# Performance work log

Measured on AMD Instinct MI355X. Metric: run time of the kernel, lower is better.

## Reference

```python
import jax, jax.numpy as jnp
import numpy as np

B, G, D, H, KD = 32, 512, 128, 4, 32  # batch, graph, embed_dim, n_heads, key_dim=embed//heads
NORM = 1.0 / np.sqrt(KD).astype(np.float32)  # MultiHeadCompat norm_factor = 1/sqrt(key_dim)


def _uniform(k, shape, fan):
    s = 1.0 / np.sqrt(fan).astype(np.float32)
    return jax.random.uniform(k, shape, jnp.float32, -s, s)


def setup_inputs() -> dict:
    key = jax.random.key(0)
    ks = jax.random.split(key, 16)
    inp = {
        "h": jax.random.normal(ks[0], (B, G, D), jnp.float32),
        "pos_pickup": jax.random.randint(ks[1], (B,), 0, G),
        "pos_delivery": jax.random.randint(ks[2], (B,), 0, G),
        "rec": jax.random.randint(ks[3], (B, G), 0, G),
        # compater_insert1 / compater_insert2 projections: (n_heads, input_dim, key_dim)
        "Wq1": _uniform(ks[4], (H, D, KD), KD),
        "Wk1": _uniform(ks[5], (H, D, KD), KD),
        "Wq2": _uniform(ks[6], (H, D, KD), KD),
        "Wk2": _uniform(ks[7], (H, D, KD), KD),
        # agg MLP(16, 32, 32, 1); stored as (in, out) so y = x @ W + b
        "fc1_w": _uniform(ks[8], (16, 32), 16),
        "fc1_b": _uniform(ks[9], (32,), 32),
        "fc2_w": _uniform(ks[10], (32, 32), 32),
        "fc2_b": _uniform(ks[11], (32,), 32),
        "fc3_w": _uniform(ks[12], (32, 1), 32),
        "fc3_b": _uniform(ks[13], (1,), 1),
    }
    return inp


def _compat(qv, hh, Wq, Wk):
    # qv: (B, D) single query node; hh: (B, G, D)
    Q = jnp.einsum('bd,hdk->bhk', qv, Wq)       # (B, H, K)
    K = jnp.einsum('bgd,hdk->bhgk', hh, Wk)     # (B, H, G, K)
    return NORM * jnp.einsum('bhk,bhgk->bgh', Q, K)  # (B, G, H)


def reference(h, pos_pickup, pos_delivery, rec, Wq1, Wk1, Wq2, Wk2,
              fc1_w, fc1_b, fc2_w, fc2_b, fc3_w, fc3_b):
    b, g, d = h.shape
    ar = jnp.arange(b)
    h_pickup = h[ar, pos_pickup]      # (B, D)
    h_delivery = h[ar, pos_delivery]  # (B, D)
    h_neighbour = jnp.take_along_axis(h, rec[:, :, None], axis=1)  # (B, G, D)

    shp = (b, g, g, 4)
    c_pp = jnp.broadcast_to(_compat(h_pickup, h, Wq1, Wk1)[:, :, None, :], shp)
    c_po = jnp.broadcast_to(_compat(h_pickup, h_neighbour, Wq2, Wk2)[:, :, None, :], shp)
    c_dp = jnp.broadcast_to(_compat(h_delivery, h, Wq1, Wk1)[:, None, :, :], shp)
    c_do = jnp.broadcast_to(_compat(h_delivery, h_neighbour, Wq2, Wk2)[:, None, :, :], shp)
    x = jnp.concatenate([c_pp, c_po, c_dp, c_do], axis=-1)  # (B, G, G, 16)

    # agg MLP (dropout p=0.05 is identity at inference)
    x = jax.nn.relu(x @ fc1_w + fc1_b)
    x = jax.nn.relu(x @ fc2_w + fc2_b)
    return (x @ fc3_w + fc3_b)[..., 0]  # (B, G, G)
```

## Files before the change

kernel.cpp:

```cpp
#include <hip/hip_runtime.h>


#define B 32
#define G 512
#define D 128
#define NH 4
#define KD 32
#define NORMF 0.17677669529663687f

#define WS_BIASF 1024
#define WS_W3F   1056
#define WS_P16H  131072
#define WS_Q16H  655360

typedef float v16f __attribute__((ext_vector_type(16)));
typedef float f2v __attribute__((ext_vector_type(2)));
typedef _Float16 v8h __attribute__((ext_vector_type(8)));
typedef _Float16 h2v __attribute__((ext_vector_type(2)));

struct HQ { h2v h[4]; };
struct F2x8 { f2v v[8]; };

__device__ __forceinline__ v8h relu_add(const HQ& p, const HQ& q) {
  const h2v z = {(_Float16)0.0f, (_Float16)0.0f};
  HQ r;
#pragma unroll
  for (int i = 0; i < 4; ++i)
    r.h[i] = __builtin_elementwise_max(p.h[i] + q.h[i], z);
  return __builtin_bit_cast(v8h, r);
}

__global__ __launch_bounds__(256) void stage01(
    const float* __restrict__ h, const int* __restrict__ pp,
    const int* __restrict__ pd, const int* __restrict__ rec,
    const float* __restrict__ Wq1, const float* __restrict__ Wk1,
    const float* __restrict__ Wq2, const float* __restrict__ Wk2,
    const float* __restrict__ fc1_w, const float* __restrict__ fc1_b,
    const float* __restrict__ fc2_w, const float* __restrict__ fc2_b,
    const float* __restrict__ fc3_w,
    float* __restrict__ ws) {
  const int bx = blockIdx.x;
  const int b = bx >> 3, g0 = (bx & 7) * 64;
  const int t = threadIdx.x;

  if (bx == 0 && t < 32) {
    _Float16* wt = (_Float16*)ws;
#pragma unroll
    for (int k = 0; k < 32; ++k) wt[t * 32 + k] = (_Float16)fc2_w[k * 32 + t];
    const int r = t & 15, hf = t >> 4;
    const int n = (r & 3) + 8 * (r >> 2) + 4 * hf;
    ws[WS_BIASF + t] = fc2_b[n];
    ws[WS_W3F + t]   = fc3_w[n];
  }

  __shared__ float hp[D], hd[D];
  __shared__ float qq[4][NH * KD];
  __shared__ float sA[4][NH][D];
  __shared__ float sc[64][17];
  __shared__ float sout[64][33];
  __shared__ float sout2[64][33];

  if (t < 128) {
    hp[t] = h[((size_t)b * G + pp[b]) * D + t];
  } else {
    const int u = t - 128;
    hd[u] = h[((size_t)b * G + pd[b]) * D + u];
  }
  __syncthreads();

  if (t < 128) {
    const int hh = t >> 5, k = t & 31;
    const float* wq1 = Wq1 + hh * D * KD + k;
    const float* wq2 = Wq2 + hh * D * KD + k;
    float s1p = 0.f, s2p = 0.f, s1d = 0.f, s2d = 0.f;
#pragma unroll 8
    for (int d = 0; d < D; ++d) {
      const float w1 = wq1[d * KD], w2 = wq2[d * KD];
      const float xp = hp[d], xd = hd[d];
      s1p = fmaf(xp, w1, s1p);
      s2p = fmaf(xp, w2, s2p);
      s1d = fmaf(xd, w1, s1d);
      s2d = fmaf(xd, w2, s2d);
    }
    qq[0][t] = s1p; qq[1][t] = s2p; qq[2][t] = s1d; qq[3][t] = s2d;
  }
  __syncthreads();

  {
    const int d = t & 127;
    const int h0 = (t >> 7) * 2;
#pragma unroll
    for (int hh = h0; hh < h0 + 2; ++hh) {
      const float* wk1 = Wk1 + hh * D * KD + d * KD;
      const float* wk2 = Wk2 + hh * D * KD + d * KD;
      float apq = 0.f, apo = 0.f, adp = 0.f, ado = 0.f;
#pragma unroll
      for (int k = 0; k < KD; ++k) {
        const float w1 = wk1[k], w2 = wk2[k];
        apq = fmaf(qq[0][hh * 32 + k], w1, apq);
        adp = fmaf(qq[2][hh * 32 + k], w1, adp);
        apo = fmaf(qq[1][hh * 32 + k], w2, apo);
        ado = fmaf(qq[3][hh * 32 + k], w2, ado);
      }
      sA[0][hh][d] = NORMF * apq;
      sA[1][hh][d] = NORMF * apo;
      sA[2][hh][d] = NORMF * adp;
      sA[3][hh][d] = NORMF * ado;
    }
  }
  __syncthreads();

  const int gl = t & 63;
  const int hh = __builtin_amdgcn_readfirstlane(t >> 6);
  const int g = g0 + gl;
  const float4* hg4 = (const float4*)(h + ((size_t)b * G + g) * D);
  const float4* hn4 = (const float4*)(h + ((size_t)b * G + rec[b * G + g]) * D);

  float cpp = 0.f, cpo = 0.f, cdp = 0.f, cdo = 0.f;
#pragma unroll 4
  for (int d4 = 0; d4 < 32; ++d4) {
    const float4 x = hg4[d4], y = hn4[d4];
    const float4 a1 = *(const float4*)&sA[0][hh][4 * d4];
    const float4 a2 = *(const float4*)&sA[1][hh][4 * d4];
    const float4 a3 = *(const float4*)&sA[2][hh][4 * d4];
    const float4 a4 = *(const float4*)&sA[3][hh][4 * d4];
    cpp = fmaf(x.x, a1.x, fmaf(x.y, a1.y, fmaf(x.z, a1.z, fmaf(x.w, a1.w, cpp))));
    cpo = fmaf(y.x, a2.x, fmaf(y.y, a2.y, fmaf(y.z, a2.z, fmaf(y.w, a2.w, cpo))));
    cdp = fmaf(x.x, a3.x, fmaf(x.y, a3.y, fmaf(x.z, a3.z, fmaf(x.w, a3.w, cdp))));
    cdo = fmaf(y.x, a4.x, fmaf(y.y, a4.y, fmaf(y.z, a4.z, fmaf(y.w, a4.w, cdo))));
  }
  sc[gl][hh] = cpp; sc[gl][4 + hh] = cpo; sc[gl][8 + hh] = cdp; sc[gl][12 + hh] = cdo;
  __syncthreads();

  float u[16];
#pragma unroll
  for (int i = 0; i < 16; ++i) u[i] = sc[gl][i];

  float pv[8], qv[8];
#pragma unroll
  for (int jj = 0; jj < 8; ++jj) {
    const int j = hh * 8 + jj;
    float p = 0.f, q = fc1_b[j];
#pragma unroll
    for (int i = 0; i < 8; ++i) {
      p = fmaf(u[i], fc1_w[i * 32 + j], p);
      q = fmaf(u[8 + i], fc1_w[(8 + i) * 32 + j], q);
    }
    pv[jj] = p; qv[jj] = q;
  }

#pragma unroll
  for (int jj = 0; jj < 8; ++jj) {
    sout[gl][hh * 8 + jj]  = pv[jj];
    sout2[gl][hh * 8 + jj] = qv[jj];
  }
  __syncthreads();
  {
    unsigned* dstP = (unsigned*)((unsigned short*)ws + WS_P16H) +
                     ((size_t)b * G + g0) * 16;
    unsigned* dstQ = (unsigned*)((unsigned short*)ws + WS_Q16H) +
                     ((size_t)b * G + g0) * 16;
#pragma unroll
    for (int i = t; i < 1024; i += 256) {
      const int row = i >> 4, c0 = (2 * i) & 31;
      __fp16 __attribute__((ext_vector_type(2))) pk =
          __builtin_amdgcn_cvt_pkrtz(sout[row][c0], sout[row][c0 + 1]);
      dstP[i] = *(const unsigned*)&pk;
      __fp16 __attribute__((ext_vector_type(2))) qk =
          __builtin_amdgcn_cvt_pkrtz(sout2[row][c0], sout2[row][c0 + 1]);
      dstQ[i] = *(const unsigned*)&qk;
    }
  }
}

__global__ __launch_bounds__(256, 2) void mlp_pairs(
    const float* __restrict__ ws, const float* __restrict__ fc3_b,
    float* __restrict__ out) {
  const int b = blockIdx.z;
  const int g1_0 = blockIdx.y * 16;
  const int g2_0 = blockIdx.x * 256;
  const int t = threadIdx.x;
  const int w = t >> 6, l = t & 63;
  const int col = l & 31;
  const int half = l >> 5;
  const int kb = half * 8;

  __shared__ __align__(16) unsigned short sPh[16 * 32];
  {
    const unsigned* Psrc = (const unsigned*)((const unsigned short*)ws + WS_P16H) +
                           ((size_t)b * G + g1_0) * 16;
    ((unsigned*)sPh)[t] = Psrc[t];
  }

  const unsigned short* wt = (const unsigned short*)ws;
  const v8h A0 = __builtin_bit_cast(v8h, *(const uint4*)(wt + col * 32 + kb));
  const v8h A1 = __builtin_bit_cast(v8h, *(const uint4*)(wt + col * 32 + 16 + kb));
  const v16f biasC = *(const v16f*)(ws + WS_BIASF + half * 16);
  const F2x8 w3p = __builtin_bit_cast(F2x8, *(const v16f*)(ws + WS_W3F + half * 16));
  const float b3h = 0.5f * fc3_b[0];

  HQ qlo[2], qhi[2];
#pragma unroll
  for (int c = 0; c < 2; ++c) {
    const unsigned short* qp = (const unsigned short*)ws + WS_Q16H +
        ((size_t)b * G + g2_0 + (2 * w + c) * 32 + col) * 32;
    qlo[c] = __builtin_bit_cast(HQ, *(const uint4*)(qp + kb));
    qhi[c] = __builtin_bit_cast(HQ, *(const uint4*)(qp + 16 + kb));
  }
  __syncthreads();

  const f2v binit = {b3h, 0.f};
  const f2v z2 = {0.f, 0.f};
  float* op = out + (((size_t)b * G + g1_0) * G) + g2_0 + w * 64 + half * 32 + col;
#pragma unroll 4
  for (int i = 0; i < 8; ++i) {
    const int ra = 2 * i, rb = 2 * i + 1;
    const HQ palo = __builtin_bit_cast(HQ, *(const uint4*)(sPh + ra * 32 + kb));
    const HQ pahi = __builtin_bit_cast(HQ, *(const uint4*)(sPh + ra * 32 + 16 + kb));
    const HQ pblo = __builtin_bit_cast(HQ, *(const uint4*)(sPh + rb * 32 + kb));
    const HQ pbhi = __builtin_bit_cast(HQ, *(const uint4*)(sPh + rb * 32 + 16 + kb));

    const v8h Ba0lo = relu_add(palo, qlo[0]);
    const v8h Ba0hi = relu_add(pahi, qhi[0]);
    const v8h Ba1lo = relu_add(palo, qlo[1]);
    const v8h Ba1hi = relu_add(pahi, qhi[1]);
    const v8h Bb0lo = relu_add(pblo, qlo[0]);
    const v8h Bb0hi = relu_add(pbhi, qhi[0]);
    const v8h Bb1lo = relu_add(pblo, qlo[1]);
    const v8h Bb1hi = relu_add(pbhi, qhi[1]);

    v16f aa0 = __builtin_amdgcn_mfma_f32_32x32x16_f16(A0, Ba0lo, biasC, 0, 0, 0);
    v16f aa1 = __builtin_amdgcn_mfma_f32_32x32x16_f16(A0, Ba1lo, biasC, 0, 0, 0);
    v16f ab0 = __builtin_amdgcn_mfma_f32_32x32x16_f16(A0, Bb0lo, biasC, 0, 0, 0);
    v16f ab1 = __builtin_amdgcn_mfma_f32_32x32x16_f16(A0, Bb1lo, biasC, 0, 0, 0);
    aa0 = __builtin_amdgcn_mfma_f32_32x32x16_f16(A1, Ba0hi, aa0, 0, 0, 0);
    aa1 = __builtin_amdgcn_mfma_f32_32x32x16_f16(A1, Ba1hi, aa1, 0, 0, 0);
    ab0 = __builtin_amdgcn_mfma_f32_32x32x16_f16(A1, Bb0hi, ab0, 0, 0, 0);
    ab1 = __builtin_amdgcn_mfma_f32_32x32x16_f16(A1, Bb1hi, ab1, 0, 0, 0);

    const F2x8 fa0 = __builtin_bit_cast(F2x8, aa0);
    const F2x8 fa1 = __builtin_bit_cast(F2x8, aa1);
    const F2x8 fb0 = __builtin_bit_cast(F2x8, ab0);
    const F2x8 fb1 = __builtin_bit_cast(F2x8, ab1);
    f2v ea0a = binit, ea1a = binit, eb0a = binit, eb1a = binit;
    f2v ea0b = z2, ea1b = z2, eb0b = z2, eb1b = z2;
#pragma unroll
    for (int k = 0; k < 4; ++k) {
      ea0a = __builtin_elementwise_max(fa0.v[k], z2) * w3p.v[k] + ea0a;
      ea1a = __builtin_elementwise_max(fa1.v[k], z2) * w3p.v[k] + ea1a;
      eb0a = __builtin_elementwise_max(fb0.v[k], z2) * w3p.v[k] + eb0a;
      eb1a = __builtin_elementwise_max(fb1.v[k], z2) * w3p.v[k] + eb1a;
      ea0b = __builtin_elementwise_max(fa0.v[k + 4], z2) * w3p.v[k + 4] + ea0b;
      ea1b = __builtin_elementwise_max(fa1.v[k + 4], z2) * w3p.v[k + 4] + ea1b;
      eb0b = __builtin_elementwise_max(fb0.v[k + 4], z2) * w3p.v[k + 4] + eb0b;
      eb1b = __builtin_elementwise_max(fb1.v[k + 4], z2) * w3p.v[k + 4] + eb1b;
    }
    const f2v ea0 = ea0a + ea0b, ea1 = ea1a + ea1b;
    const f2v eb0 = eb0a + eb0b, eb1 = eb1a + eb1b;
    const float sa0 = ea0[0] + ea0[1], sa1 = ea1[0] + ea1[1];
    const float sb0 = eb0[0] + eb0[1], sb1 = eb1[0] + eb1[1];

    float ya = half ? sa1 : sa0;
    float za = half ? sa0 : sa1;
    ya += __shfl_xor(za, 32);
    float yb = half ? sb1 : sb0;
    float zb = half ? sb0 : sb1;
    yb += __shfl_xor(zb, 32);

    op[(size_t)ra * G] = ya;
    op[(size_t)rb * G] = yb;
  }
}

extern "C" void kernel_launch(void* const* d_in, const int* in_sizes, int n_in,
                              void* d_out, int out_size, void* d_ws, size_t ws_size,
                              hipStream_t stream) {
  const float* h     = (const float*)d_in[0];
  const int*   pp    = (const int*)d_in[1];
  const int*   pd    = (const int*)d_in[2];
  const int*   rec   = (const int*)d_in[3];
  const float* Wq1   = (const float*)d_in[4];
  const float* Wk1   = (const float*)d_in[5];
  const float* Wq2   = (const float*)d_in[6];
  const float* Wk2   = (const float*)d_in[7];
  const float* fc1_w = (const float*)d_in[8];
  const float* fc1_b = (const float*)d_in[9];
  const float* fc2_w = (const float*)d_in[10];
  const float* fc2_b = (const float*)d_in[11];
  const float* fc3_w = (const float*)d_in[12];
  const float* fc3_b = (const float*)d_in[13];
  float* out = (float*)d_out;
  float* ws  = (float*)d_ws;

  stage01<<<dim3(256), dim3(256), 0, stream>>>(
      h, pp, pd, rec, Wq1, Wk1, Wq2, Wk2, fc1_w, fc1_b, fc2_w, fc2_b, fc3_w, ws);
  mlp_pairs<<<dim3(2, 32, 32), dim3(256), 0, stream>>>(ws, fc3_b, out);
}
```

Measured before the change: 147.0 us.

## Split stage01 into per-batch projection kernel and wider per-node compat kernel

The old first kernel recomputed the per-batch query/key projection (the A vectors) in each of its 8 blocks per batch. That work now runs once per (batch, head) in a separate stage0 kernel that writes A to the workspace. A new stage1 kernel uses 512 blocks of 32 nodes each, giving more parallelism and less redundant work. The cost is one extra kernel launch plus a round trip of A through global memory, and workspace offsets are shifted to make room.

```diff
diff --git a/kernel.cpp b/kernel.cpp
--- a/kernel.cpp
+++ b/kernel.cpp
@@ -10,8 +10,9 @@
 
 #define WS_BIASF 1024
 #define WS_W3F   1056
-#define WS_P16H  131072
-#define WS_Q16H  655360
+#define WS_AF    4096
+#define WS_P16H  262144
+#define WS_Q16H  786432
 
 typedef float v16f __attribute__((ext_vector_type(16)));
 typedef float f2v __attribute__((ext_vector_type(2)));
@@ -30,17 +31,16 @@
   return __builtin_bit_cast(v8h, r);
 }
 
-__global__ __launch_bounds__(256) void stage01(
+__global__ __launch_bounds__(256) void stage0(
     const float* __restrict__ h, const int* __restrict__ pp,
-    const int* __restrict__ pd, const int* __restrict__ rec,
+    const int* __restrict__ pd,
     const float* __restrict__ Wq1, const float* __restrict__ Wk1,
     const float* __restrict__ Wq2, const float* __restrict__ Wk2,
-    const float* __restrict__ fc1_w, const float* __restrict__ fc1_b,
     const float* __restrict__ fc2_w, const float* __restrict__ fc2_b,
     const float* __restrict__ fc3_w,
     float* __restrict__ ws) {
   const int bx = blockIdx.x;
-  const int b = bx >> 3, g0 = (bx & 7) * 64;
+  const int b = bx >> 2, hh = bx & 3;
   const int t = threadIdx.x;
 
   if (bx == 0 && t < 32) {
@@ -54,11 +54,8 @@
   }
 
   __shared__ float hp[D], hd[D];
-  __shared__ float qq[4][NH * KD];
-  __shared__ float sA[4][NH][D];
-  __shared__ float sc[64][17];
-  __shared__ float sout[64][33];
-  __shared__ float sout2[64][33];
+  __shared__ float qpart[4][2][KD];
+  __shared__ float qq[4 * KD];
 
   if (t < 128) {
     hp[t] = h[((size_t)b * G + pp[b]) * D + t];
@@ -68,106 +65,119 @@
   }
   __syncthreads();
 
-  if (t < 128) {
-    const int hh = t >> 5, k = t & 31;
-    const float* wq1 = Wq1 + hh * D * KD + k;
-    const float* wq2 = Wq2 + hh * D * KD + k;
-    float s1p = 0.f, s2p = 0.f, s1d = 0.f, s2d = 0.f;
+  {
+    const int s = t >> 6;
+    const int dh = (t >> 5) & 1;
+    const int k = t & 31;
+    const float* xs = (s & 2) ? hd : hp;
+    const float* wq = ((s & 1) ? Wq2 : Wq1) + hh * D * KD + k;
+    float acc = 0.f;
 #pragma unroll 8
-    for (int d = 0; d < D; ++d) {
-      const float w1 = wq1[d * KD], w2 = wq2[d * KD];
-      const float xp = hp[d], xd = hd[d];
-      s1p = fmaf(xp, w1, s1p);
-      s2p = fmaf(xp, w2, s2p);
-      s1d = fmaf(xd, w1, s1d);
-      s2d = fmaf(xd, w2, s2d);
-    }
-    qq[0][t] = s1p; qq[1][t] = s2p; qq[2][t] = s1d; qq[3][t] = s2d;
-  }
+    for (int i = 0; i < 64; ++i) {
+      const int d = dh * 64 + i;
+      acc = fmaf(xs[d], wq[d * KD], acc);
+    }
+    qpart[s][dh][k] = acc;
+  }
+  __syncthreads();
+  if (t < 128) qq[t] = qpart[t >> 5][0][t & 31] + qpart[t >> 5][1][t & 31];
   __syncthreads();
 
   {
     const int d = t & 127;
-    const int h0 = (t >> 7) * 2;
-#pragma unroll
-    for (int hh = h0; hh < h0 + 2; ++hh) {
-      const float* wk1 = Wk1 + hh * D * KD + d * KD;
-      const float* wk2 = Wk2 + hh * D * KD + d * KD;
-      float apq = 0.f, apo = 0.f, adp = 0.f, ado = 0.f;
-#pragma unroll
-      for (int k = 0; k < KD; ++k) {
-        const float w1 = wk1[k], w2 = wk2[k];
-        apq = fmaf(qq[0][hh * 32 + k], w1, apq);
-        adp = fmaf(qq[2][hh * 32 + k], w1, adp);
-        apo = fmaf(qq[1][hh * 32 + k], w2, apo);
-        ado = fmaf(qq[3][hh * 32 + k], w2, ado);
-      }
-      sA[0][hh][d] = NORMF * apq;
-      sA[1][hh][d] = NORMF * apo;
-      sA[2][hh][d] = NORMF * adp;
-      sA[3][hh][d] = NORMF * ado;
-    }
-  }
-  __syncthreads();
-
-  const int gl = t & 63;
-  const int hh = __builtin_amdgcn_readfirstlane(t >> 6);
+    const int ps = t >> 7;
+    const float* wk = (ps ? Wk2 : Wk1) + hh * D * KD + d * KD;
+    const float* q0 = qq + (ps ? 1 : 0) * KD;
+    const float* q1 = qq + (ps ? 3 : 2) * KD;
+    float a0 = 0.f, a1 = 0.f;
+#pragma unroll
+    for (int k = 0; k < KD; ++k) {
+      const float wv = wk[k];
+      a0 = fmaf(q0[k], wv, a0);
+      a1 = fmaf(q1[k], wv, a1);
+    }
+    float* A = ws + WS_AF + (size_t)b * 2048;
+    A[((ps)     * 4 + hh) * 128 + d] = NORMF * a0;
+    A[((ps + 2) * 4 + hh) * 128 + d] = NORMF * a1;
+  }
+}
+
+__global__ __launch_bounds__(256) void stage1(
+    const float* __restrict__ h, const int* __restrict__ rec,
+    const float* __restrict__ fc1_w, const float* __restrict__ fc1_b,
+    float* __restrict__ ws) {
+  const int bx = blockIdx.x;
+  const int b = bx >> 4, g0 = (bx & 15) * 32;
+  const int t = threadIdx.x;
+
+  __shared__ float sA[16][128];
+  __shared__ float sc[32][17];
+  __shared__ float sout[32][33];
+  __shared__ float sout2[32][33];
+
+  {
+    const float4* src = (const float4*)(ws + WS_AF + (size_t)b * 2048);
+    float4* dst = (float4*)&sA[0][0];
+    dst[t] = src[t];
+    dst[t + 256] = src[t + 256];
+  }
+  __syncthreads();
+
+  const int gl = t & 31;
+  const int sel = t >> 5;
+  const int hh = sel & 3, pidx = sel >> 2;
   const int g = g0 + gl;
-  const float4* hg4 = (const float4*)(h + ((size_t)b * G + g) * D);
-  const float4* hn4 = (const float4*)(h + ((size_t)b * G + rec[b * G + g]) * D);
-
-  float cpp = 0.f, cpo = 0.f, cdp = 0.f, cdo = 0.f;
+  const int row = pidx ? rec[b * G + g] : g;
+  const float4* x4 = (const float4*)(h + ((size_t)b * G + row) * D);
+  const float* A0 = &sA[(pidx ? 1 : 0) * 4 + hh][0];
+  const float* A1 = &sA[(pidx ? 3 : 2) * 4 + hh][0];
+
+  float c0 = 0.f, c1 = 0.f;
 #pragma unroll 4
   for (int d4 = 0; d4 < 32; ++d4) {
-    const float4 x = hg4[d4], y = hn4[d4];
-    const float4 a1 = *(const float4*)&sA[0][hh][4 * d4];
-    const float4 a2 = *(const float4*)&sA[1][hh][4 * d4];
-    const float4 a3 = *(const float4*)&sA[2][hh][4 * d4];
-    const float4 a4 = *(const float4*)&sA[3][hh][4 * d4];
-    cpp = fmaf(x.x, a1.x, fmaf(x.y, a1.y, fmaf(x.z, a1.z, fmaf(x.w, a1.w, cpp))));
-    cpo = fmaf(y.x, a2.x, fmaf(y.y, a2.y, fmaf(y.z, a2.z, fmaf(y.w, a2.w, cpo))));
-    cdp = fmaf(x.x, a3.x, fmaf(x.y, a3.y, fmaf(x.z, a3.z, fmaf(x.w, a3.w, cdp))));
-    cdo = fmaf(y.x, a4.x, fmaf(y.y, a4.y, fmaf(y.z, a4.z, fmaf(y.w, a4.w, cdo))));
-  }
-  sc[gl][hh] = cpp; sc[gl][4 + hh] = cpo; sc[gl][8 + hh] = cdp; sc[gl][12 + hh] = cdo;
-  __syncthreads();
-
-  float u[16];
-#pragma unroll
-  for (int i = 0; i < 16; ++i) u[i] = sc[gl][i];
-
-  float pv[8], qv[8];
-#pragma unroll
-  for (int jj = 0; jj < 8; ++jj) {
-    const int j = hh * 8 + jj;
-    float p = 0.f, q = fc1_b[j];
-#pragma unroll
-    for (int i = 0; i < 8; ++i) {
-      p = fmaf(u[i], fc1_w[i * 32 + j], p);
-      q = fmaf(u[8 + i], fc1_w[(8 + i) * 32 + j], q);
-    }
-    pv[jj] = p; qv[jj] = q;
-  }
-
-#pragma unroll
-  for (int jj = 0; jj < 8; ++jj) {
-    sout[gl][hh * 8 + jj]  = pv[jj];
-    sout2[gl][hh * 8 + jj] = qv[jj];
-  }
-  __syncthreads();
+    const float4 x = x4[d4];
+    const float4 a = *(const float4*)&A0[4 * d4];
+    const float4 bb = *(const float4*)&A1[4 * d4];
+    c0 = fmaf(x.x, a.x, fmaf(x.y, a.y, fmaf(x.z, a.z, fmaf(x.w, a.w, c0))));
+    c1 = fmaf(x.x, bb.x, fmaf(x.y, bb.y, fmaf(x.z, bb.z, fmaf(x.w, bb.w, c1))));
+  }
+  sc[gl][(pidx ? 4 : 0) + hh] = c0;
+  sc[gl][(pidx ? 12 : 8) + hh] = c1;
+  __syncthreads();
+
+  {
+    float u[16];
+#pragma unroll
+    for (int i = 0; i < 16; ++i) u[i] = sc[gl][i];
+    const int jb = (t >> 5) * 4;
+#pragma unroll
+    for (int jj = 0; jj < 4; ++jj) {
+      const int j = jb + jj;
+      float p = 0.f, q = fc1_b[j];
+#pragma unroll
+      for (int i = 0; i < 8; ++i) {
+        p = fmaf(u[i], fc1_w[i * 32 + j], p);
+        q = fmaf(u[8 + i], fc1_w[(8 + i) * 32 + j], q);
+      }
+      sout[gl][j] = p;
+      sout2[gl][j] = q;
+    }
+  }
+  __syncthreads();
+
   {
     unsigned* dstP = (unsigned*)((unsigned short*)ws + WS_P16H) +
                      ((size_t)b * G + g0) * 16;
     unsigned* dstQ = (unsigned*)((unsigned short*)ws + WS_Q16H) +
                      ((size_t)b * G + g0) * 16;
 #pragma unroll
-    for (int i = t; i < 1024; i += 256) {
-      const int row = i >> 4, c0 = (2 * i) & 31;
+    for (int i = t; i < 512; i += 256) {
+      const int row2 = i >> 4, c0i = (2 * i) & 31;
       __fp16 __attribute__((ext_vector_type(2))) pk =
-          __builtin_amdgcn_cvt_pkrtz(sout[row][c0], sout[row][c0 + 1]);
+          __builtin_amdgcn_cvt_pkrtz(sout[row2][c0i], sout[row2][c0i + 1]);
       dstP[i] = *(const unsigned*)&pk;
       __fp16 __attribute__((ext_vector_type(2))) qk =
-          __builtin_amdgcn_cvt_pkrtz(sout2[row][c0], sout2[row][c0 + 1]);
+          __builtin_amdgcn_cvt_pkrtz(sout2[row2][c0i], sout2[row2][c0i + 1]);
       dstQ[i] = *(const unsigned*)&qk;
     }
   }
@@ -292,7 +302,8 @@
   float* out = (float*)d_out;
   float* ws  = (float*)d_ws;
 
-  stage01<<<dim3(256), dim3(256), 0, stream>>>(
-      h, pp, pd, rec, Wq1, Wk1, Wq2, Wk2, fc1_w, fc1_b, fc2_w, fc2_b, fc3_w, ws);
+  stage0<<<dim3(128), dim3(256), 0, stream>>>(
+      h, pp, pd, Wq1, Wk1, Wq2, Wk2, fc2_w, fc2_b, fc3_w, ws);
+  stage1<<<dim3(512), dim3(256), 0, stream>>>(h, rec, fc1_w, fc1_b, ws);
   mlp_pairs<<<dim3(2, 32, 32), dim3(256), 0, stream>>>(ws, fc3_b, out);
 }
```

After: 140.3 us. 1.05x faster.
